# Performance work log

Measured on AMD Instinct MI355X. Metric: run time of the kernel, lower is better.

Reference implementation:

```python
import jax, jax.numpy as jnp
import numpy as np
from jax import lax

# QConv2d: conv2d implemented in the original via unfold + quantized matmul
# with a dequantization scale. High-precision path math:
#   out = scale * conv2d(x, weight) + bias
# We express the im2col+GEMM as the mathematically identical conv.

STRIDE = (1, 1)
PADDING = ((1, 1), (1, 1))


def setup_inputs() -> dict:
    key = jax.random.key(0)
    k1, k2, k3 = jax.random.split(key, 3)
    N, C, H, W = 16, 32, 256, 256
    O, KH, KW = 32, 3, 3
    x = jax.random.normal(k1, (N, C, H, W), dtype=jnp.float32)
    weight = jax.random.normal(k2, (O, C, KH, KW), dtype=jnp.float32) * 0.1
    bias = jax.random.normal(k3, (O,), dtype=jnp.float32)
    scale = jnp.float32(0.0078125)  # quantization dequant scale (1/128)
    return {"x": x, "weight": weight, "bias": bias, "scale": scale}


def reference(x, weight, bias, scale):
    # conv2d (NCHW / OIHW), stride 1, padding 1 -> same spatial size
    out = lax.conv_general_dilated(
        x, weight,
        window_strides=STRIDE,
        padding=PADDING,
        dimension_numbers=("NCHW", "OIHW", "NCHW"),
    )
    # scale applied by the quantized matmul kernel, then bias
    return out * scale + bias[None, :, None, None]
```

## Files before the change

kernel.cpp:

```cpp
#include <hip/hip_runtime.h>

typedef unsigned short u16;
typedef unsigned int   u32;
typedef short s8v  __attribute__((ext_vector_type(8)));
typedef float f16v __attribute__((ext_vector_type(16)));
typedef unsigned int u32x4 __attribute__((ext_vector_type(4)));

#define ROWBYTES 4224
#define NROWS    10
#define LDS_BYTES (NROWS * ROWBYTES)

__device__ inline u16 f2bf(float f) {
    u32 u = __builtin_bit_cast(u32, f);
    u += 0x7FFFu + ((u >> 16) & 1u);
    return (u16)(u >> 16);
}
__device__ inline u32 pk2(float lo, float hi) {
    return (u32)f2bf(lo) | ((u32)f2bf(hi) << 16);
}

__global__ __launch_bounds__(256, 2) void k_fused(const float* __restrict__ x,
                                                  const float* __restrict__ wgt,
                                                  const float* __restrict__ bias,
                                                  const float* __restrict__ scale_p,
                                                  float* __restrict__ out) {
    __shared__ __align__(16) char lds[LDS_BYTES];

    const int b    = ((blockIdx.x & 7) << 8) | (blockIdx.x >> 3);
    const int wb   = b & 3;
    const int hs   = (b >> 2) & 31;
    const int n    = b >> 7;
    const int w0   = wb << 6;
    const int h0   = hs << 3;
    const int t    = threadIdx.x;
    const int l    = t & 63;
    const int wave = t >> 6;
    const int g    = l >> 5;
    const int ln   = l & 31;

    {
        u16* wl = (u16*)lds;
        #pragma unroll
        for (int k = 0; k < 36; ++k) {
            const int idx = t + (k << 8);
            const int tap = idx % 9;
            const int oc  = idx / 9;
            wl[tap * 1024 + oc] = f2bf(wgt[idx]);
        }
    }
    __syncthreads();

    s8v A[9][2];
    {
        const u16* wl = (const u16*)lds;
        #pragma unroll
        for (int tap = 0; tap < 9; ++tap)
            #pragma unroll
            for (int q = 0; q < 2; ++q)
                A[tap][q] = *(const s8v*)(wl + tap * 1024 + ln * 32 + q * 16 + g * 8);
    }
    const float scale = scale_p[0];
    float bias_r[16];
    #pragma unroll
    for (int rg = 0; rg < 16; ++rg) bias_r[rg] = bias[(rg & 3) + 8 * (rg >> 2) + 4 * g];
    __syncthreads();

    const float* xbase = x + ((size_t)n << 21);

    if (t < 80) {
        const int r    = t % 10;
        const int side = (t / 10) & 1;
        const int cc   = t / 20;
        const int hin  = h0 - 1 + r;
        const int wg   = w0 - 1 + side * 65;
        u32 q0 = 0, q1 = 0, q2 = 0, q3 = 0;
        if (hin >= 0 && hin < 256 && wg >= 0 && wg < 256) {
            const float* p = xbase + (size_t)(cc * 8) * 65536 + (size_t)hin * 256 + wg;
            q0 = pk2(p[0],      p[65536]);
            q1 = pk2(p[131072], p[196608]);
            q2 = pk2(p[262144], p[327680]);
            q3 = pk2(p[393216], p[458752]);
        }
        *(u32x4*)(lds + r * ROWBYTES + cc * 1056 + side * 1040) = u32x4{q0, q1, q2, q3};
    }

    {
        const float* pb = xbase + (size_t)(wave * 8) * 65536 + w0 + l;
        char* ldst = lds + wave * 1056 + ((l + 1) << 4);
        float v[NROWS][8];
        if (h0 != 0 && h0 != 248) {
            #pragma unroll
            for (int r = 0; r < NROWS; ++r) {
                const float* p = pb + (size_t)(h0 - 1 + r) * 256;
                #pragma unroll
                for (int c = 0; c < 8; ++c) v[r][c] = p[(size_t)c * 65536];
            }
            #pragma unroll
            for (int r = 0; r < NROWS; ++r) {
                *(u32x4*)(ldst + r * ROWBYTES) = u32x4{
                    pk2(v[r][0], v[r][1]), pk2(v[r][2], v[r][3]),
                    pk2(v[r][4], v[r][5]), pk2(v[r][6], v[r][7])};
            }
        } else {
            #pragma unroll
            for (int r = 0; r < NROWS; ++r) {
                const int hin = h0 - 1 + r;
                const int hcl = hin < 0 ? 0 : (hin > 255 ? 255 : hin);
                const float* p = pb + (size_t)hcl * 256;
                #pragma unroll
                for (int c = 0; c < 8; ++c) v[r][c] = p[(size_t)c * 65536];
            }
            #pragma unroll
            for (int r = 0; r < NROWS; ++r) {
                const int hin = h0 - 1 + r;
                const bool bad = (hin < 0) || (hin > 255);
                #pragma unroll
                for (int c = 0; c < 8; ++c) v[r][c] = bad ? 0.f : v[r][c];
                *(u32x4*)(ldst + r * ROWBYTES) = u32x4{
                    pk2(v[r][0], v[r][1]), pk2(v[r][2], v[r][3]),
                    pk2(v[r][4], v[r][5]), pk2(v[r][6], v[r][7])};
            }
        }
    }
    __syncthreads();

    #pragma unroll
    for (int i = 0; i < 2; ++i) {
        const int hr = (wave << 1) + i;

        f16v acc0, acc1;
        #pragma unroll
        for (int rg = 0; rg < 16; ++rg) { acc0[rg] = 0.f; acc1[rg] = 0.f; }

        #pragma unroll
        for (int kh = 0; kh < 3; ++kh) {
            const char* rowp = lds + (hr + kh) * ROWBYTES + g * 1056 + (ln << 4);
            #pragma unroll
            for (int kw = 0; kw < 3; ++kw) {
                const int tap = kh * 3 + kw;
                #pragma unroll
                for (int q = 0; q < 2; ++q) {
                    const char* pB = rowp + q * 2112 + (kw << 4);
                    const s8v b0 = *(const s8v*)pB;
                    const s8v b1 = *(const s8v*)(pB + 512);
                    acc0 = __builtin_amdgcn_mfma_f32_32x32x16_bf16(A[tap][q], b0, acc0, 0, 0, 0);
                    acc1 = __builtin_amdgcn_mfma_f32_32x32x16_bf16(A[tap][q], b1, acc1, 0, 0, 0);
                }
            }
        }

        const int h = h0 + hr;
        float* op = out + ((size_t)n << 21) + (size_t)h * 256 + w0 + ln;
        #pragma unroll
        for (int rg = 0; rg < 16; ++rg) {
            const int o = (rg & 3) + 8 * (rg >> 2) + 4 * g;
            op[(size_t)o * 65536]      = scale * acc0[rg] + bias_r[rg];
            op[(size_t)o * 65536 + 32] = scale * acc1[rg] + bias_r[rg];
        }
    }
}

extern "C" void kernel_launch(void* const* d_in, const int* in_sizes, int n_in,
                              void* d_out, int out_size, void* d_ws, size_t ws_size,
                              hipStream_t stream) {
    const float* x     = (const float*)d_in[0];
    const float* wgt   = (const float*)d_in[1];
    const float* bias  = (const float*)d_in[2];
    const float* scale = (const float*)d_in[3];
    float* out = (float*)d_out;
    k_fused<<<dim3(2048), dim3(256), 0, stream>>>(x, wgt, bias, scale, out);
}
```

Before: 61.85 us.

## Make conv kernel persistent with double-buffered LDS row tiles and prefetch

Switches to 256 blocks of 512 threads. Each block processes four consecutive 16-row strips and double-buffers the bf16 input tiles in LDS, issuing global loads for the next strip before computing the current one. This is meant to hide global load latency behind the MFMA work and to cut halo reloads and per-block weight setup. In exchange it uses much more LDS per block (about 152KB), which likely limits residency to one block per CU, and only 256 blocks are launched, which may underfill the GPU. It also holds 72 prefetched floats per thread in registers, raising register pressure.

```diff
diff --git a/kernel.cpp b/kernel.cpp
--- a/kernel.cpp
+++ b/kernel.cpp
@@ -7,8 +7,9 @@
 typedef unsigned int u32x4 __attribute__((ext_vector_type(4)));
 
 #define ROWBYTES 4224
-#define NROWS    10
-#define LDS_BYTES (NROWS * ROWBYTES)
+#define NROWS    18
+#define TILEB    (NROWS * ROWBYTES)
+#define NT       4
 
 __device__ inline u16 f2bf(float f) {
     u32 u = __builtin_bit_cast(u32, f);
@@ -19,30 +20,32 @@
     return (u32)f2bf(lo) | ((u32)f2bf(hi) << 16);
 }
 
-__global__ __launch_bounds__(256, 2) void k_fused(const float* __restrict__ x,
+__global__ __launch_bounds__(512, 2) void k_fused(const float* __restrict__ x,
                                                   const float* __restrict__ wgt,
                                                   const float* __restrict__ bias,
                                                   const float* __restrict__ scale_p,
                                                   float* __restrict__ out) {
-    __shared__ __align__(16) char lds[LDS_BYTES];
+    __shared__ __align__(16) char lds[2 * TILEB];
 
-    const int b    = ((blockIdx.x & 7) << 8) | (blockIdx.x >> 3);
-    const int wb   = b & 3;
-    const int hs   = (b >> 2) & 31;
-    const int n    = b >> 7;
-    const int w0   = wb << 6;
-    const int h0   = hs << 3;
+    const int bid     = blockIdx.x;
+    const int logical = ((bid & 7) << 5) | (bid >> 3);
+    const int n   = logical >> 4;
+    const int hsq = (logical >> 2) & 3;
+    const int wb  = logical & 3;
+    const int w0  = wb << 6;
     const int t    = threadIdx.x;
     const int l    = t & 63;
     const int wave = t >> 6;
     const int g    = l >> 5;
     const int ln   = l & 31;
+    const int chunk = wave & 3;
+    const int half  = wave >> 2;
 
     {
         u16* wl = (u16*)lds;
         #pragma unroll
-        for (int k = 0; k < 36; ++k) {
-            const int idx = t + (k << 8);
+        for (int k = 0; k < 18; ++k) {
+            const int idx = t + (k << 9);
             const int tap = idx % 9;
             const int oc  = idx / 9;
             wl[tap * 1024 + oc] = f2bf(wgt[idx]);
@@ -66,96 +69,116 @@
     __syncthreads();
 
     const float* xbase = x + ((size_t)n << 21);
+    const float* pb    = xbase + (size_t)(chunk * 8) * 65536 + w0 + l;
 
-    if (t < 80) {
-        const int r    = t % 10;
-        const int side = (t / 10) & 1;
-        const int cc   = t / 20;
-        const int hin  = h0 - 1 + r;
-        const int wg   = w0 - 1 + side * 65;
-        u32 q0 = 0, q1 = 0, q2 = 0, q3 = 0;
-        if (hin >= 0 && hin < 256 && wg >= 0 && wg < 256) {
-            const float* p = xbase + (size_t)(cc * 8) * 65536 + (size_t)hin * 256 + wg;
-            q0 = pk2(p[0],      p[65536]);
-            q1 = pk2(p[131072], p[196608]);
-            q2 = pk2(p[262144], p[327680]);
-            q3 = pk2(p[393216], p[458752]);
+    float v[9][8];
+    float hv[8];
+
+    auto issueA = [&](int hs) {
+        const int h0 = hs << 4;
+        #pragma unroll
+        for (int j = 0; j < 9; ++j) {
+            const int hin = h0 - 1 + half + (j << 1);
+            const int hcl = hin < 0 ? 0 : (hin > 255 ? 255 : hin);
+            const float* p = pb + (size_t)hcl * 256;
+            #pragma unroll
+            for (int c = 0; c < 8; ++c) v[j][c] = p[(size_t)c * 65536];
         }
-        *(u32x4*)(lds + r * ROWBYTES + cc * 1056 + side * 1040) = u32x4{q0, q1, q2, q3};
-    }
+        if (t < 144) {
+            const int cc = t / 36, rem = t - cc * 36, side = rem / 18, r = rem - side * 18;
+            const int hin = h0 - 1 + r;
+            const int hcl = hin < 0 ? 0 : (hin > 255 ? 255 : hin);
+            const int wg  = w0 - 1 + side * 65;
+            const int wcl = wg < 0 ? 0 : (wg > 255 ? 255 : wg);
+            const float* p = xbase + (size_t)(cc * 8) * 65536 + (size_t)hcl * 256 + wcl;
+            #pragma unroll
+            for (int c = 0; c < 8; ++c) hv[c] = p[(size_t)c * 65536];
+        }
+    };
 
-    {
-        const float* pb = xbase + (size_t)(wave * 8) * 65536 + w0 + l;
-        char* ldst = lds + wave * 1056 + ((l + 1) << 4);
-        float v[NROWS][8];
-        if (h0 != 0 && h0 != 248) {
+    auto writeC = [&](int hs, char* buf) {
+        const int h0 = hs << 4;
+        #pragma unroll
+        for (int j = 0; j < 9; ++j) {
+            const int hin = h0 - 1 + half + (j << 1);
+            const bool bad = (hin < 0) || (hin > 255);
             #pragma unroll
-            for (int r = 0; r < NROWS; ++r) {
-                const float* p = pb + (size_t)(h0 - 1 + r) * 256;
+            for (int c = 0; c < 8; ++c) v[j][c] = bad ? 0.f : v[j][c];
+        }
+        char* ldst = buf + chunk * 1056 + ((l + 1) << 4);
+        #pragma unroll
+        for (int j = 0; j < 9; ++j) {
+            const int r = half + (j << 1);
+            *(u32x4*)(ldst + r * ROWBYTES) = u32x4{
+                pk2(v[j][0], v[j][1]), pk2(v[j][2], v[j][3]),
+                pk2(v[j][4], v[j][5]), pk2(v[j][6], v[j][7])};
+        }
+        if (t < 144) {
+            const int cc = t / 36, rem = t - cc * 36, side = rem / 18, r = rem - side * 18;
+            const int hin = h0 - 1 + r;
+            const int wg  = w0 - 1 + side * 65;
+            const bool bad = (hin < 0) || (hin > 255) || (wg < 0) || (wg > 255);
+            #pragma unroll
+            for (int c = 0; c < 8; ++c) hv[c] = bad ? 0.f : hv[c];
+            *(u32x4*)(buf + r * ROWBYTES + cc * 1056 + side * 1040) = u32x4{
+                pk2(hv[0], hv[1]), pk2(hv[2], hv[3]),
+                pk2(hv[4], hv[5]), pk2(hv[6], hv[7])};
+        }
+    };
+
+    auto compute = [&](int hs, const char* buf) {
+        const int h0 = hs << 4;
+        #pragma unroll
+        for (int i = 0; i < 2; ++i) {
+            const int hr = (wave << 1) + i;
+
+            f16v acc0, acc1;
+            #pragma unroll
+            for (int rg = 0; rg < 16; ++rg) { acc0[rg] = 0.f; acc1[rg] = 0.f; }
+
+            #pragma unroll
+            for (int kh = 0; kh < 3; ++kh) {
+                const char* rowp = buf + (hr + kh) * ROWBYTES + g * 1056 + (ln << 4);
                 #pragma unroll
-                for (int c = 0; c < 8; ++c) v[r][c] = p[(size_t)c * 65536];
+                for (int kw = 0; kw < 3; ++kw) {
+                    const int tap = kh * 3 + kw;
+                    #pragma unroll
+                    for (int q = 0; q < 2; ++q) {
+                        const char* pB = rowp + q * 2112 + (kw << 4);
+                        const s8v b0 = *(const s8v*)pB;
+                        const s8v b1 = *(const s8v*)(pB + 512);
+                        acc0 = __builtin_amdgcn_mfma_f32_32x32x16_bf16(A[tap][q], b0, acc0, 0, 0, 0);
+                        acc1 = __builtin_amdgcn_mfma_f32_32x32x16_bf16(A[tap][q], b1, acc1, 0, 0, 0);
+                    }
+                }
             }
+
+            const int h = h0 + hr;
+            float* op = out + ((size_t)n << 21) + (size_t)h * 256 + w0 + ln;
             #pragma unroll
-            for (int r = 0; r < NROWS; ++r) {
-                *(u32x4*)(ldst + r * ROWBYTES) = u32x4{
-                    pk2(v[r][0], v[r][1]), pk2(v[r][2], v[r][3]),
-                    pk2(v[r][4], v[r][5]), pk2(v[r][6], v[r][7])};
-            }
-        } else {
-            #pragma unroll
-            for (int r = 0; r < NROWS; ++r) {
-                const int hin = h0 - 1 + r;
-                const int hcl = hin < 0 ? 0 : (hin > 255 ? 255 : hin);
-                const float* p = pb + (size_t)hcl * 256;
-                #pragma unroll
-                for (int c = 0; c < 8; ++c) v[r][c] = p[(size_t)c * 65536];
-            }
-            #pragma unroll
-            for (int r = 0; r < NROWS; ++r) {
-                const int hin = h0 - 1 + r;
-                const bool bad = (hin < 0) || (hin > 255);
-                #pragma unroll
-                for (int c = 0; c < 8; ++c) v[r][c] = bad ? 0.f : v[r][c];
-                *(u32x4*)(ldst + r * ROWBYTES) = u32x4{
-                    pk2(v[r][0], v[r][1]), pk2(v[r][2], v[r][3]),
-                    pk2(v[r][4], v[r][5]), pk2(v[r][6], v[r][7])};
+            for (int rg = 0; rg < 16; ++rg) {
+                const int o = (rg & 3) + 8 * (rg >> 2) + 4 * g;
+                op[(size_t)o * 65536]      = scale * acc0[rg] + bias_r[rg];
+                op[(size_t)o * 65536 + 32] = scale * acc1[rg] + bias_r[rg];
             }
         }
-    }
+    };
+
+    const int hs0 = hsq << 2;
+    issueA(hs0);
+    writeC(hs0, lds);
     __syncthreads();
 
     #pragma unroll
-    for (int i = 0; i < 2; ++i) {
-        const int hr = (wave << 1) + i;
-
-        f16v acc0, acc1;
-        #pragma unroll
-        for (int rg = 0; rg < 16; ++rg) { acc0[rg] = 0.f; acc1[rg] = 0.f; }
-
-        #pragma unroll
-        for (int kh = 0; kh < 3; ++kh) {
-            const char* rowp = lds + (hr + kh) * ROWBYTES + g * 1056 + (ln << 4);
-            #pragma unroll
-            for (int kw = 0; kw < 3; ++kw) {
-                const int tap = kh * 3 + kw;
-                #pragma unroll
-                for (int q = 0; q < 2; ++q) {
-                    const char* pB = rowp + q * 2112 + (kw << 4);
-                    const s8v b0 = *(const s8v*)pB;
-                    const s8v b1 = *(const s8v*)(pB + 512);
-                    acc0 = __builtin_amdgcn_mfma_f32_32x32x16_bf16(A[tap][q], b0, acc0, 0, 0, 0);
-                    acc1 = __builtin_amdgcn_mfma_f32_32x32x16_bf16(A[tap][q], b1, acc1, 0, 0, 0);
-                }
-            }
-        }
-
-        const int h = h0 + hr;
-        float* op = out + ((size_t)n << 21) + (size_t)h * 256 + w0 + ln;
-        #pragma unroll
-        for (int rg = 0; rg < 16; ++rg) {
-            const int o = (rg & 3) + 8 * (rg >> 2) + 4 * g;
-            op[(size_t)o * 65536]      = scale * acc0[rg] + bias_r[rg];
-            op[(size_t)o * 65536 + 32] = scale * acc1[rg] + bias_r[rg];
+    for (int tt = 0; tt < NT; ++tt) {
+        char* cur = lds + (tt & 1) * TILEB;
+        char* nxt = lds + ((tt + 1) & 1) * TILEB;
+        if (tt < NT - 1) issueA(hs0 + tt + 1);
+        __builtin_amdgcn_sched_barrier(0);
+        compute(hs0 + tt, cur);
+        if (tt < NT - 1) {
+            writeC(hs0 + tt + 1, nxt);
+            __syncthreads();
         }
     }
 }
@@ -168,5 +191,5 @@
     const float* bias  = (const float*)d_in[2];
     const float* scale = (const float*)d_in[3];
     float* out = (float*)d_out;
-    k_fused<<<dim3(2048), dim3(256), 0, stream>>>(x, wgt, bias, scale, out);
+    k_fused<<<dim3(256), dim3(512), 0, stream>>>(x, wgt, bias, scale, out);
 }
```

Result: slower. 71.71 us (+15.9%).
